# Optimization experiments

Hardware: AMD Instinct MI355X
Metric: run time of the kernel (lower is better)

## Reference

```python
import jax, jax.numpy as jnp
import numpy as np

NUM_CLASSES = 16
IOU_TH = 0.5
SCORE_TH = 0.05
MAX_DET = 100
MAX_PER_CLASS = 100


def setup_inputs() -> dict:
    key = jax.random.key(0)
    kxy, kwh, kc, ks = jax.random.split(key, 4)
    B, N = 4, 2048
    # xyxy boxes inside a ~640x640 image
    xy = jax.random.uniform(kxy, (B, N, 2), dtype=jnp.float32) * 576.0
    wh = jax.random.uniform(kwh, (B, N, 2), dtype=jnp.float32) * 56.0 + 8.0
    cls = jax.random.randint(kc, (B, N), 0, NUM_CLASSES).astype(jnp.float32)
    score = jax.random.uniform(ks, (B, N), dtype=jnp.float32)
    predictions = jnp.concatenate(
        [xy, xy + wh, cls[..., None], score[..., None]], axis=-1
    )  # [B, N, 6] = (x1, y1, x2, y2, class, confidence)
    return {"predictions": predictions}


def _pairwise_iou(b):
    # b: [N, 4] in yxyx
    y1, x1, y2, x2 = b[:, 0], b[:, 1], b[:, 2], b[:, 3]
    area = (y2 - y1) * (x2 - x1)
    ih = jnp.clip(jnp.minimum(y2[:, None], y2[None, :]) - jnp.maximum(y1[:, None], y1[None, :]), 0.0)
    iw = jnp.clip(jnp.minimum(x2[:, None], x2[None, :]) - jnp.maximum(x1[:, None], x1[None, :]), 0.0)
    inter = ih * iw
    union = area[:, None] + area[None, :] - inter
    return jnp.where(inter > 0.0, inter / jnp.maximum(union, 1e-8), 0.0)


def _per_image(boxes, cls_id, score):
    # boxes: [N, 4] yxyx, cls_id: [N] int32, score: [N]
    N = boxes.shape[0]
    iou = _pairwise_iou(boxes)  # [N, N], shared across classes
    idx_r = jnp.arange(N)

    def per_class(c):
        # one-hot scoring: only boxes labelled c have nonzero score for class c
        sc = jnp.where(cls_id == c, score, 0.0)
        order = jnp.argsort(-sc)
        s = sc[order]
        b = boxes[order]
        iou_s = iou[order][:, order]
        valid = s > SCORE_TH

        def body(i, keep):
            sup = (iou_s[i] > IOU_TH) & (idx_r > i)
            return jnp.where(keep[i], keep & ~sup, keep)

        keep = jax.lax.fori_loop(0, N, body, valid)  # greedy suppression
        masked = jnp.where(keep, s, -1.0)
        top_s, top_i = jax.lax.top_k(masked, MAX_PER_CLASS)
        vmask = top_s > SCORE_TH
        return b[top_i], jnp.where(vmask, top_s, 0.0), vmask

    cb, cs, cv = jax.lax.map(per_class, jnp.arange(NUM_CLASSES))
    cb = cb.reshape(-1, 4)
    cs = cs.reshape(-1)
    cv = cv.reshape(-1)
    ccls = jnp.repeat(jnp.arange(NUM_CLASSES, dtype=jnp.float32), MAX_PER_CLASS)
    # merge per-class detections, keep global top MAX_DET by score
    top_s, top_i = jax.lax.top_k(jnp.where(cv, cs, -1.0), MAX_DET)
    vmask = top_s > SCORE_TH
    out_b = jnp.where(vmask[:, None], cb[top_i], 0.0)
    out_c = jnp.where(vmask, ccls[top_i], 0.0)
    out_s = jnp.where(vmask, top_s, 0.0)
    return out_b, out_c, out_s, jnp.sum(vmask.astype(jnp.int32))


def reference(predictions):
    # convert xyxy -> yxyx (pure coordinate permutation)
    boxes_yxyx = predictions[..., :4][..., jnp.array([1, 0, 3, 2])]
    cls_id = predictions[..., 4].astype(jnp.int32)
    score = predictions[..., 5]
    ob, oc, os, nvalid = jax.vmap(_per_image)(boxes_yxyx, cls_id, score)
    # convert kept boxes back yxyx -> xyxy, re-attach class and confidence.
    # Original layer returns a ragged tensor; we return the padded equivalent
    # [B, MAX_DET, 6] plus per-image valid counts (the ragged row lengths).
    ob_xyxy = ob[..., jnp.array([1, 0, 3, 2])]
    out = jnp.concatenate([ob_xyxy, oc[..., None], os[..., None]], axis=-1)
    return out, nvalid
```

## Files before the change

kernel.cpp:

```cpp
#include <hip/hip_runtime.h>

#define NMS_NUM_CLASSES 16
#define NMS_N 2048
#define NMS_IOU_TH 0.5f
#define NMS_SCORE_TH 0.05f
#define NMS_MAX_DET 100
#define NMS_MAX_PER_CLASS 100
#define NMS_NS (NMS_NUM_CLASSES * NMS_MAX_PER_CLASS)
#define NMS_TILE 128


__device__ __forceinline__ int nms_cmp(float sj, int ij, float sq, int iq) {
    return ((int)(sj > sq)) | (((int)(sj == sq)) & ((int)(ij < iq)));
}

__global__ __launch_bounds__(1024) void nms_per_class_kernel(
    const float* __restrict__ pred,
    float* __restrict__ ws_scores,
    float* __restrict__ ws_boxes,
    float* __restrict__ out,
    int B)
{
    const int b = blockIdx.x / NMS_NUM_CLASSES;
    const int c = blockIdx.x % NMS_NUM_CLASSES;
    const float* p = pred + (size_t)b * NMS_N * 6;
    const int tid = threadIdx.x;
    const int lane = tid & 63;
    const int w = tid >> 6;

    if (c == 0) {
        float* ob = out + (size_t)b * NMS_MAX_DET * 6;
        for (int t = tid; t < NMS_MAX_DET * 6; t += 1024) ob[t] = 0.0f;
        if (tid == 0) out[(size_t)B * NMS_MAX_DET * 6 + b] = 0.0f;
    }

    __shared__ float s_scu[NMS_N];
    __shared__ int   s_ixu[NMS_N];
    __shared__ float s_bxu[NMS_N * 4];
    __shared__ int   s_rk[NMS_N];
    __shared__ float s_sc[NMS_N];
    __shared__ float s_bx[NMS_N * 4];
    __shared__ unsigned char s_keep[NMS_N];
    __shared__ unsigned int s_supc[4 * NMS_TILE];
    __shared__ int s_m;

    if (tid == 0) s_m = 0;
    __syncthreads();

    const float2* p2 = (const float2*)p;
    for (int i = tid; i < NMS_N; i += 1024) {
        s_rk[i] = 0;
        float2 v0 = p2[i * 3 + 0];
        float2 v1 = p2[i * 3 + 1];
        float2 v2 = p2[i * 3 + 2];
        const bool ok = ((int)v2.x == c) && (v2.y > NMS_SCORE_TH);
        unsigned long long mask = __ballot(ok);
        int base = 0;
        if (lane == 0) {
            int cnt = __popcll(mask);
            if (cnt) base = atomicAdd(&s_m, cnt);
        }
        base = __shfl(base, 0, 64);
        if (ok) {
            int pos = base + __popcll(mask & ((1ull << lane) - 1ull));
            s_scu[pos] = v2.y;
            s_ixu[pos] = i;
            s_bxu[pos * 4 + 0] = v0.x;
            s_bxu[pos * 4 + 1] = v0.y;
            s_bxu[pos * 4 + 2] = v1.x;
            s_bxu[pos * 4 + 3] = v1.y;
        }
    }
    __syncthreads();
    const int M = s_m;

    {
        const int nch = (M + 31) >> 5;
        const int ntask = M * nch;
        for (int task = tid; task < ntask; task += 1024) {
            const int q = task % M;
            const int ch = task / M;
            const float sq = s_scu[q];
            const int   iq = s_ixu[q];
            const int j0 = ch << 5;
            int jend = j0 + 32; if (jend > M) jend = M;
            int r0 = 0, r1 = 0, r2 = 0, r3 = 0;
            int j = j0;
            for (; j + 4 <= jend; j += 4) {
                float sa = s_scu[j + 0], sb = s_scu[j + 1];
                float sc2 = s_scu[j + 2], sd = s_scu[j + 3];
                int ia = s_ixu[j + 0], ib = s_ixu[j + 1];
                int ic = s_ixu[j + 2], id = s_ixu[j + 3];
                r0 += nms_cmp(sa, ia, sq, iq);
                r1 += nms_cmp(sb, ib, sq, iq);
                r2 += nms_cmp(sc2, ic, sq, iq);
                r3 += nms_cmp(sd, id, sq, iq);
            }
            for (; j < jend; ++j)
                r0 += nms_cmp(s_scu[j], s_ixu[j], sq, iq);
            const int rk = (r0 + r1) + (r2 + r3);
            if (rk) atomicAdd(&s_rk[q], rk);
        }
    }
    __syncthreads();
    for (int q = tid; q < M; q += 1024) {
        int rk = s_rk[q];
        s_sc[rk] = s_scu[q];
        s_bx[rk * 4 + 0] = s_bxu[q * 4 + 0];
        s_bx[rk * 4 + 1] = s_bxu[q * 4 + 1];
        s_bx[rk * 4 + 2] = s_bxu[q * 4 + 2];
        s_bx[rk * 4 + 3] = s_bxu[q * 4 + 3];
        s_keep[rk] = 1;
    }
    __syncthreads();

    for (int t0 = 0; t0 < M; t0 += NMS_TILE) {
        const int tm = (M - t0 < NMS_TILE) ? (M - t0) : NMS_TILE;

        if (t0 > 0) {
            for (int jj = tid; jj < tm; jj += 1024) {
                const int gj = t0 + jj;
                float jx1 = s_bx[gj * 4 + 0], jy1 = s_bx[gj * 4 + 1];
                float jx2 = s_bx[gj * 4 + 2], jy2 = s_bx[gj * 4 + 3];
                float aj = (jy2 - jy1) * (jx2 - jx1);
                int dead = 0;
                for (int i = 0; i < t0 && !dead; ++i) {
                    if (!s_keep[i]) continue;
                    float ix1 = s_bx[i * 4 + 0], iy1 = s_bx[i * 4 + 1];
                    float ix2 = s_bx[i * 4 + 2], iy2 = s_bx[i * 4 + 3];
                    float ai = (iy2 - iy1) * (ix2 - ix1);
                    float ih = fminf(iy2, jy2) - fmaxf(iy1, jy1);
                    ih = fmaxf(ih, 0.0f);
                    float iw = fminf(ix2, jx2) - fmaxf(ix1, jx1);
                    iw = fmaxf(iw, 0.0f);
                    float inter = ih * iw;
                    float uni = ai + aj - inter;
                    float iou = (inter > 0.0f) ? inter / fmaxf(uni, 1e-08f) : 0.0f;
                    dead = iou > NMS_IOU_TH;
                }
                if (dead) s_keep[gj] = 0;
            }
            __syncthreads();
        }

        for (int idx = tid; idx < 4 * tm; idx += 1024) {
            const int wi = idx / tm;
            const int jj = idx % tm;
            const int ibase = wi << 5;
            unsigned int m0 = 0, m1 = 0, m2 = 0, m3 = 0;
            int iend = jj - ibase;
            if (iend > 32) iend = 32;
            if (iend > 0) {
                const int gj = t0 + jj;
                float jx1 = s_bx[gj * 4 + 0], jy1 = s_bx[gj * 4 + 1];
                float jx2 = s_bx[gj * 4 + 2], jy2 = s_bx[gj * 4 + 3];
                float aj = (jy2 - jy1) * (jx2 - jx1);
                int bb = 0;
                for (; bb + 4 <= iend; bb += 4) {
#define NMS_SUP1(K, MK)                                                        \
                    {                                                          \
                        const int gi = t0 + ibase + bb + (K);                  \
                        float ix1 = s_bx[gi * 4 + 0], iy1 = s_bx[gi * 4 + 1];  \
                        float ix2 = s_bx[gi * 4 + 2], iy2 = s_bx[gi * 4 + 3];  \
                        float ai = (iy2 - iy1) * (ix2 - ix1);                  \
                        float ih = fminf(iy2, jy2) - fmaxf(iy1, jy1);          \
                        ih = fmaxf(ih, 0.0f);                                  \
                        float iw = fminf(ix2, jx2) - fmaxf(ix1, jx1);          \
                        iw = fmaxf(iw, 0.0f);                                  \
                        float inter = ih * iw;                                 \
                        float uni = ai + aj - inter;                           \
                        float iou = (inter > 0.0f) ? inter / fmaxf(uni, 1e-08f) : 0.0f; \
                        MK |= (iou > NMS_IOU_TH) ? (1u << (bb + (K))) : 0u;    \
                    }
                    NMS_SUP1(0, m0)
                    NMS_SUP1(1, m1)
                    NMS_SUP1(2, m2)
                    NMS_SUP1(3, m3)
                }
                for (; bb < iend; ++bb) {
                    const int gi = t0 + ibase + bb;
                    float ix1 = s_bx[gi * 4 + 0], iy1 = s_bx[gi * 4 + 1];
                    float ix2 = s_bx[gi * 4 + 2], iy2 = s_bx[gi * 4 + 3];
                    float ai = (iy2 - iy1) * (ix2 - ix1);
                    float ih = fminf(iy2, jy2) - fmaxf(iy1, jy1);
                    ih = fmaxf(ih, 0.0f);
                    float iw = fminf(ix2, jx2) - fmaxf(ix1, jx1);
                    iw = fmaxf(iw, 0.0f);
                    float inter = ih * iw;
                    float uni = ai + aj - inter;
                    float iou = (inter > 0.0f) ? inter / fmaxf(uni, 1e-08f) : 0.0f;
                    m0 |= (iou > NMS_IOU_TH) ? (1u << bb) : 0u;
                }
#undef NMS_SUP1
            }
            s_supc[wi * NMS_TILE + jj] = (m0 | m1) | (m2 | m3);
        }
        __syncthreads();

        if (w == 0) {
            const int j0 = lane, j1 = lane + 64;
            const bool h0 = j0 < tm, h1 = j1 < tm;
            unsigned int m00 = 0, m01 = 0, m02 = 0, m03 = 0;
            unsigned int m10 = 0, m11 = 0, m12 = 0, m13 = 0;
            int ext0 = 0, ext1 = 0;
            if (h0) {
                m00 = s_supc[0 * NMS_TILE + j0];
                m01 = s_supc[1 * NMS_TILE + j0];
                m02 = s_supc[2 * NMS_TILE + j0];
                m03 = s_supc[3 * NMS_TILE + j0];
                ext0 = (int)s_keep[t0 + j0];
            }
            if (h1) {
                m10 = s_supc[0 * NMS_TILE + j1];
                m11 = s_supc[1 * NMS_TILE + j1];
                m12 = s_supc[2 * NMS_TILE + j1];
                m13 = s_supc[3 * NMS_TILE + j1];
                ext1 = (int)s_keep[t0 + j1];
            }
            int alive0 = ext0, alive1 = ext1;
            for (int round = 0; round < NMS_TILE; ++round) {
                unsigned long long A0b = __ballot(alive0 != 0);
                unsigned long long A1b = __ballot(alive1 != 0);
                const unsigned int kw0 = (unsigned int)(A0b & 0xffffffffu);
                const unsigned int kw1 = (unsigned int)(A0b >> 32);
                const unsigned int kw2 = (unsigned int)(A1b & 0xffffffffu);
                const unsigned int kw3 = (unsigned int)(A1b >> 32);
                int na0 = 0, na1 = 0;
                if (ext0)
                    na0 = (((m00 & kw0) | (m01 & kw1) | (m02 & kw2) | (m03 & kw3)) == 0u);
                if (ext1)
                    na1 = (((m10 & kw0) | (m11 & kw1) | (m12 & kw2) | (m13 & kw3)) == 0u);
                const unsigned long long chg =
                    __ballot(na0 != alive0) | __ballot(na1 != alive1);
                alive0 = na0; alive1 = na1;
                if (chg == 0ull) break;
            }
            if (h0) s_keep[t0 + j0] = (unsigned char)alive0;
            if (h1) s_keep[t0 + j1] = (unsigned char)alive1;
        }
        __syncthreads();
    }

    if (w == 0) {
        const int chunk = (M + 63) >> 6;
        int lo = lane * chunk;
        int hi = lo + chunk; if (hi > M) hi = M;
        int cnt2 = 0;
        for (int jj = lo; jj < hi; ++jj) cnt2 += s_keep[jj];
        int inc2 = cnt2;
        for (int off = 1; off < 64; off <<= 1) {
            int n = __shfl_up(inc2, off, 64);
            if (lane >= off) inc2 += n;
        }
        int epos = inc2 - cnt2;
        const int total = __shfl(inc2, 63, 64);

        float* osc = ws_scores + ((size_t)b * NMS_NUM_CLASSES + c) * NMS_MAX_PER_CLASS;
        float* obx = ws_boxes + (((size_t)b * NMS_NUM_CLASSES + c) * NMS_MAX_PER_CLASS) * 4;
        for (int jj = lo; jj < hi; ++jj) {
            if (s_keep[jj]) {
                if (epos < NMS_MAX_PER_CLASS) {
                    osc[epos] = s_sc[jj];
                    obx[epos * 4 + 0] = s_bx[jj * 4 + 0];
                    obx[epos * 4 + 1] = s_bx[jj * 4 + 1];
                    obx[epos * 4 + 2] = s_bx[jj * 4 + 2];
                    obx[epos * 4 + 3] = s_bx[jj * 4 + 3];
                }
                epos++;
            }
        }
        for (int pp = lane; pp < NMS_MAX_PER_CLASS; pp += 64) {
            if (pp >= total) osc[pp] = -1.0f;
        }
    }
}

__global__ __launch_bounds__(1024) void nms_topk_kernel(
    const float* __restrict__ ws_scores,
    const float* __restrict__ ws_boxes,
    float* __restrict__ out,
    int B)
{
    const int b = blockIdx.x / NMS_NUM_CLASSES;
    const int c = blockIdx.x % NMS_NUM_CLASSES;
    const int cbase = c * NMS_MAX_PER_CLASS;
    __shared__ float s_sc[NMS_NS];
    __shared__ int s_rank[NMS_MAX_PER_CLASS];

    const float* isc = ws_scores + (size_t)b * NMS_NS;
    for (int t = threadIdx.x; t < NMS_NS; t += blockDim.x) s_sc[t] = isc[t];
    if (threadIdx.x < NMS_MAX_PER_CLASS) s_rank[threadIdx.x] = 0;
    __syncthreads();

    for (int task = threadIdx.x; task < NMS_MAX_PER_CLASS * 16; task += blockDim.x) {
        const int slot = task % NMS_MAX_PER_CLASS;
        const int chunk = task / NMS_MAX_PER_CLASS;
        const int flat = cbase + slot;
        const float s = s_sc[flat];
        const int j0 = chunk * 100;
        int r0 = 0, r1 = 0, r2 = 0, r3 = 0;
        for (int j = j0; j < j0 + 100; j += 4) {
            float sa = s_sc[j + 0], sb = s_sc[j + 1];
            float sc2 = s_sc[j + 2], sd = s_sc[j + 3];
            r0 += ((int)(sa > s)) | (((int)(sa == s)) & ((int)(j + 0 < flat)));
            r1 += ((int)(sb > s)) | (((int)(sb == s)) & ((int)(j + 1 < flat)));
            r2 += ((int)(sc2 > s)) | (((int)(sc2 == s)) & ((int)(j + 2 < flat)));
            r3 += ((int)(sd > s)) | (((int)(sd == s)) & ((int)(j + 3 < flat)));
        }
        const int rk = (r0 + r1) + (r2 + r3);
        if (rk) atomicAdd(&s_rank[slot], rk);
    }
    __syncthreads();

    int is_top = 0;
    const int t = threadIdx.x;
    if (t < NMS_MAX_PER_CLASS) {
        const int slot = cbase + t;
        float s = s_sc[slot];
        if (s > NMS_SCORE_TH) {
            int rk = s_rank[t];
            if (rk < NMS_MAX_DET) {
                const float* bx = ws_boxes + ((size_t)b * NMS_NS + slot) * 4;
                float* row = out + (size_t)b * NMS_MAX_DET * 6 + rk * 6;
                row[0] = bx[0];
                row[1] = bx[1];
                row[2] = bx[2];
                row[3] = bx[3];
                row[4] = (float)c;
                row[5] = s;
                is_top = 1;
            }
        }
    }
    unsigned long long m = __ballot(is_top);
    if ((threadIdx.x & 63) == 0) {
        float cnt = (float)__popcll(m);
        if (cnt > 0.0f)
            atomicAdd(&out[(size_t)B * NMS_MAX_DET * 6 + b], cnt);
    }
}

extern "C" void kernel_launch(void* const* d_in, const int* in_sizes, int n_in,
                              void* d_out, int out_size, void* d_ws, size_t ws_size,
                              hipStream_t stream) {
    const float* pred = (const float*)d_in[0];
    const int B = in_sizes[0] / (NMS_N * 6);
    if (B <= 0) return;
    float* out = (float*)d_out;

    float* ws_scores = (float*)d_ws;
    float* ws_boxes = ws_scores + (size_t)B * NMS_NS;

    nms_per_class_kernel<<<dim3(B * NMS_NUM_CLASSES), dim3(1024), 0, stream>>>(
        pred, ws_scores, ws_boxes, out, B);
    nms_topk_kernel<<<dim3(B * NMS_NUM_CLASSES), dim3(1024), 0, stream>>>(
        ws_scores, ws_boxes, out, B);
}
```

Measured before the change: 93.95 us.

## Replace atomic compaction with prefix-sum and use direct rank sort for small classes

Stream compaction of candidate boxes now loads both halves up front and uses a per-wave count table with a prefix sum instead of a shared atomic counter. When the class has at most 1024 candidates, each thread computes its full rank directly and scatters in place, removing the rank atomics and an extra barrier and pass. The top-k kernel skips comparing against its own class block (the self-rank is initialized instead) and processes two tasks per thread in a single pass. These changes aim to cut synchronization and atomic overhead in the short serial phases, at the cost of longer per-thread loops in the small-M path.

```diff
diff --git a/kernel.cpp b/kernel.cpp
--- a/kernel.cpp
+++ b/kernel.cpp
@@ -42,39 +42,83 @@
     __shared__ float s_bx[NMS_N * 4];
     __shared__ unsigned char s_keep[NMS_N];
     __shared__ unsigned int s_supc[4 * NMS_TILE];
-    __shared__ int s_m;
-
-    if (tid == 0) s_m = 0;
+    __shared__ int s_wcnt[16];
+
+    const float2* p2 = (const float2*)p;
+    const int iA = tid, iB = tid + 1024;
+    float2 a0 = p2[iA * 3 + 0];
+    float2 a1 = p2[iA * 3 + 1];
+    float2 a2 = p2[iA * 3 + 2];
+    float2 b0 = p2[iB * 3 + 0];
+    float2 b1 = p2[iB * 3 + 1];
+    float2 b2 = p2[iB * 3 + 2];
+    const bool okA = ((int)a2.x == c) && (a2.y > NMS_SCORE_TH);
+    const bool okB = ((int)b2.x == c) && (b2.y > NMS_SCORE_TH);
+    const unsigned long long mA = __ballot(okA);
+    const unsigned long long mB = __ballot(okB);
+    const int cA = __popcll(mA), cB = __popcll(mB);
+    if (lane == 0) s_wcnt[w] = cA + cB;
     __syncthreads();
-
-    const float2* p2 = (const float2*)p;
-    for (int i = tid; i < NMS_N; i += 1024) {
-        s_rk[i] = 0;
-        float2 v0 = p2[i * 3 + 0];
-        float2 v1 = p2[i * 3 + 1];
-        float2 v2 = p2[i * 3 + 2];
-        const bool ok = ((int)v2.x == c) && (v2.y > NMS_SCORE_TH);
-        unsigned long long mask = __ballot(ok);
-        int base = 0;
-        if (lane == 0) {
-            int cnt = __popcll(mask);
-            if (cnt) base = atomicAdd(&s_m, cnt);
-        }
-        base = __shfl(base, 0, 64);
-        if (ok) {
-            int pos = base + __popcll(mask & ((1ull << lane) - 1ull));
-            s_scu[pos] = v2.y;
-            s_ixu[pos] = i;
-            s_bxu[pos * 4 + 0] = v0.x;
-            s_bxu[pos * 4 + 1] = v0.y;
-            s_bxu[pos * 4 + 2] = v1.x;
-            s_bxu[pos * 4 + 3] = v1.y;
-        }
+    int wbase = 0, M = 0;
+    for (int ww = 0; ww < 16; ++ww) {
+        const int v = s_wcnt[ww];
+        wbase += (ww < w) ? v : 0;
+        M += v;
+    }
+    const unsigned long long below = (1ull << lane) - 1ull;
+    if (okA) {
+        const int pos = wbase + __popcll(mA & below);
+        s_scu[pos] = a2.y;
+        s_ixu[pos] = iA;
+        s_bxu[pos * 4 + 0] = a0.x;
+        s_bxu[pos * 4 + 1] = a0.y;
+        s_bxu[pos * 4 + 2] = a1.x;
+        s_bxu[pos * 4 + 3] = a1.y;
+    }
+    if (okB) {
+        const int pos = wbase + cA + __popcll(mB & below);
+        s_scu[pos] = b2.y;
+        s_ixu[pos] = iB;
+        s_bxu[pos * 4 + 0] = b0.x;
+        s_bxu[pos * 4 + 1] = b0.y;
+        s_bxu[pos * 4 + 2] = b1.x;
+        s_bxu[pos * 4 + 3] = b1.y;
     }
     __syncthreads();
-    const int M = s_m;
-
-    {
+
+    if (M <= 1024) {
+        if (tid < M) {
+            const float sq = s_scu[tid];
+            const int   iq = s_ixu[tid];
+            int r0 = 0, r1 = 0, r2 = 0, r3 = 0;
+            int j = 0;
+            for (; j + 8 <= M; j += 8) {
+                float sa = s_scu[j + 0], sb = s_scu[j + 1];
+                float sc2 = s_scu[j + 2], sd = s_scu[j + 3];
+                float se = s_scu[j + 4], sf = s_scu[j + 5];
+                float sg = s_scu[j + 6], sh = s_scu[j + 7];
+                int ia = s_ixu[j + 0], ib2 = s_ixu[j + 1];
+                int ic = s_ixu[j + 2], id = s_ixu[j + 3];
+                int ie = s_ixu[j + 4], ifx = s_ixu[j + 5];
+                int ig = s_ixu[j + 6], ih = s_ixu[j + 7];
+                r0 += nms_cmp(sa, ia, sq, iq) + nms_cmp(se, ie, sq, iq);
+                r1 += nms_cmp(sb, ib2, sq, iq) + nms_cmp(sf, ifx, sq, iq);
+                r2 += nms_cmp(sc2, ic, sq, iq) + nms_cmp(sg, ig, sq, iq);
+                r3 += nms_cmp(sd, id, sq, iq) + nms_cmp(sh, ih, sq, iq);
+            }
+            for (; j < M; ++j)
+                r0 += nms_cmp(s_scu[j], s_ixu[j], sq, iq);
+            const int rk = (r0 + r1) + (r2 + r3);
+            s_sc[rk] = sq;
+            s_bx[rk * 4 + 0] = s_bxu[tid * 4 + 0];
+            s_bx[rk * 4 + 1] = s_bxu[tid * 4 + 1];
+            s_bx[rk * 4 + 2] = s_bxu[tid * 4 + 2];
+            s_bx[rk * 4 + 3] = s_bxu[tid * 4 + 3];
+            s_keep[rk] = 1;
+        }
+    } else {
+        for (int q = tid; q < M; q += 1024) s_rk[q] = 0;
+        __syncthreads();
         const int nch = (M + 31) >> 5;
         const int ntask = M * nch;
         for (int task = tid; task < ntask; task += 1024) {
@@ -84,33 +128,21 @@
             const int   iq = s_ixu[q];
             const int j0 = ch << 5;
             int jend = j0 + 32; if (jend > M) jend = M;
-            int r0 = 0, r1 = 0, r2 = 0, r3 = 0;
-            int j = j0;
-            for (; j + 4 <= jend; j += 4) {
-                float sa = s_scu[j + 0], sb = s_scu[j + 1];
-                float sc2 = s_scu[j + 2], sd = s_scu[j + 3];
-                int ia = s_ixu[j + 0], ib = s_ixu[j + 1];
-                int ic = s_ixu[j + 2], id = s_ixu[j + 3];
-                r0 += nms_cmp(sa, ia, sq, iq);
-                r1 += nms_cmp(sb, ib, sq, iq);
-                r2 += nms_cmp(sc2, ic, sq, iq);
-                r3 += nms_cmp(sd, id, sq, iq);
-            }
-            for (; j < jend; ++j)
-                r0 += nms_cmp(s_scu[j], s_ixu[j], sq, iq);
-            const int rk = (r0 + r1) + (r2 + r3);
+            int rk = 0;
+            for (int j = j0; j < jend; ++j)
+                rk += nms_cmp(s_scu[j], s_ixu[j], sq, iq);
             if (rk) atomicAdd(&s_rk[q], rk);
         }
-    }
-    __syncthreads();
-    for (int q = tid; q < M; q += 1024) {
-        int rk = s_rk[q];
-        s_sc[rk] = s_scu[q];
-        s_bx[rk * 4 + 0] = s_bxu[q * 4 + 0];
-        s_bx[rk * 4 + 1] = s_bxu[q * 4 + 1];
-        s_bx[rk * 4 + 2] = s_bxu[q * 4 + 2];
-        s_bx[rk * 4 + 3] = s_bxu[q * 4 + 3];
-        s_keep[rk] = 1;
+        __syncthreads();
+        for (int q = tid; q < M; q += 1024) {
+            int rk = s_rk[q];
+            s_sc[rk] = s_scu[q];
+            s_bx[rk * 4 + 0] = s_bxu[q * 4 + 0];
+            s_bx[rk * 4 + 1] = s_bxu[q * 4 + 1];
+            s_bx[rk * 4 + 2] = s_bxu[q * 4 + 2];
+            s_bx[rk * 4 + 3] = s_bxu[q * 4 + 3];
+            s_keep[rk] = 1;
+        }
     }
     __syncthreads();
 
@@ -289,26 +321,46 @@
 
     const float* isc = ws_scores + (size_t)b * NMS_NS;
     for (int t = threadIdx.x; t < NMS_NS; t += blockDim.x) s_sc[t] = isc[t];
-    if (threadIdx.x < NMS_MAX_PER_CLASS) s_rank[threadIdx.x] = 0;
+    if (threadIdx.x < NMS_MAX_PER_CLASS) s_rank[threadIdx.x] = threadIdx.x;
     __syncthreads();
 
-    for (int task = threadIdx.x; task < NMS_MAX_PER_CLASS * 16; task += blockDim.x) {
-        const int slot = task % NMS_MAX_PER_CLASS;
-        const int chunk = task / NMS_MAX_PER_CLASS;
-        const int flat = cbase + slot;
-        const float s = s_sc[flat];
-        const int j0 = chunk * 100;
-        int r0 = 0, r1 = 0, r2 = 0, r3 = 0;
-        for (int j = j0; j < j0 + 100; j += 4) {
-            float sa = s_sc[j + 0], sb = s_sc[j + 1];
-            float sc2 = s_sc[j + 2], sd = s_sc[j + 3];
-            r0 += ((int)(sa > s)) | (((int)(sa == s)) & ((int)(j + 0 < flat)));
-            r1 += ((int)(sb > s)) | (((int)(sb == s)) & ((int)(j + 1 < flat)));
-            r2 += ((int)(sc2 > s)) | (((int)(sc2 == s)) & ((int)(j + 2 < flat)));
-            r3 += ((int)(sd > s)) | (((int)(sd == s)) & ((int)(j + 3 < flat)));
-        }
-        const int rk = (r0 + r1) + (r2 + r3);
-        if (rk) atomicAdd(&s_rank[slot], rk);
+    {
+        const int tA = threadIdx.x;
+        const int tB = threadIdx.x + 1024;
+        const bool hB = tB < NMS_MAX_PER_CLASS * 15;
+        const int slotA = tA % NMS_MAX_PER_CLASS;
+        const int chA0 = tA / NMS_MAX_PER_CLASS;
+        const int chA = chA0 + (chA0 >= c ? 1 : 0);
+        const int slotB = hB ? (tB % NMS_MAX_PER_CLASS) : slotA;
+        const int chB0 = hB ? (tB / NMS_MAX_PER_CLASS) : chA0;
+        const int chB = chB0 + (chB0 >= c ? 1 : 0);
+        const int flatA = cbase + slotA;
+        const int flatB = cbase + slotB;
+        const float sA = s_sc[flatA];
+        const float sB = s_sc[flatB];
+        const int jA0 = chA * 100;
+        const int jB0 = chB * 100;
+        int a0 = 0, a1 = 0, a2 = 0, a3 = 0;
+        int b0 = 0, b1 = 0, b2 = 0, b3 = 0;
+        for (int k = 0; k < 100; k += 4) {
+            const int ja = jA0 + k, jb = jB0 + k;
+            float va0 = s_sc[ja + 0], va1 = s_sc[ja + 1];
+            float va2 = s_sc[ja + 2], va3 = s_sc[ja + 3];
+            float vb0 = s_sc[jb + 0], vb1 = s_sc[jb + 1];
+            float vb2 = s_sc[jb + 2], vb3 = s_sc[jb + 3];
+            a0 += ((int)(va0 > sA)) | (((int)(va0 == sA)) & ((int)(ja + 0 < flatA)));
+            a1 += ((int)(va1 > sA)) | (((int)(va1 == sA)) & ((int)(ja + 1 < flatA)));
+            a2 += ((int)(va2 > sA)) | (((int)(va2 == sA)) & ((int)(ja + 2 < flatA)));
+            a3 += ((int)(va3 > sA)) | (((int)(va3 == sA)) & ((int)(ja + 3 < flatA)));
+            b0 += ((int)(vb0 > sB)) | (((int)(vb0 == sB)) & ((int)(jb + 0 < flatB)));
+            b1 += ((int)(vb1 > sB)) | (((int)(vb1 == sB)) & ((int)(jb + 1 < flatB)));
+            b2 += ((int)(vb2 > sB)) | (((int)(vb2 == sB)) & ((int)(jb + 2 < flatB)));
+            b3 += ((int)(vb3 > sB)) | (((int)(vb3 == sB)) & ((int)(jb + 3 < flatB)));
+        }
+        const int rkA = (a0 + a1) + (a2 + a3);
+        const int rkB = (b0 + b1) + (b2 + b3);
+        if (rkA) atomicAdd(&s_rank[slotA], rkA);
+        if (hB && rkB) atomicAdd(&s_rank[slotB], rkB);
     }
     __syncthreads();
 
```

New measurement: 101.3 us. 1.08x slower.
